# Performance work log

Hardware: AMD Instinct MI355X
Metric: run time of the kernel (lower is better)

Reference implementation:

```python
import jax, jax.numpy as jnp
import numpy as np

T_STEPS = 16
A = 64
B = 64
N = 16          # read_N
C = 3           # channels
H = 1024        # enc_size
IN = N * N * C  # LSTM input size = 768
EPS = 1e-8


def setup_inputs() -> dict:
    key = jax.random.key(0)
    ks = jax.random.split(key, 12)
    s = 0.02
    x = jax.random.normal(ks[0], (1024, C, B, A), dtype=jnp.float32)
    W_att = jax.random.normal(ks[1], (5, H), dtype=jnp.float32) * s
    b_att = jnp.zeros((5,), dtype=jnp.float32)
    W_ih = jax.random.normal(ks[2], (4 * H, IN), dtype=jnp.float32) * s
    W_hh = jax.random.normal(ks[3], (4 * H, H), dtype=jnp.float32) * s
    b_ih = jnp.zeros((4 * H,), dtype=jnp.float32)
    b_hh = jnp.zeros((4 * H,), dtype=jnp.float32)
    W_fc0 = jax.random.normal(ks[4], (H, H), dtype=jnp.float32) * s
    b_fc0 = jnp.zeros((H,), dtype=jnp.float32)
    W_fc = jax.random.normal(ks[5], (10, H), dtype=jnp.float32) * s
    b_fc = jnp.zeros((10,), dtype=jnp.float32)
    return {"x": x, "W_att": W_att, "b_att": b_att, "W_ih": W_ih, "W_hh": W_hh,
            "b_ih": b_ih, "b_hh": b_hh, "W_fc0": W_fc0, "b_fc0": b_fc0,
            "W_fc": W_fc, "b_fc": b_fc}


def _filterbank(gx, gy, sigma2, delta):
    # gx, gy, sigma2, delta: [Bt]
    grid = jnp.arange(N, dtype=jnp.float32)
    mu_x = gx[:, None] + (grid - N / 2 - 0.5) * delta[:, None]   # [Bt, N]
    mu_y = gy[:, None] + (grid - N / 2 - 0.5) * delta[:, None]   # [Bt, N]
    a = jnp.arange(A, dtype=jnp.float32)
    b = jnp.arange(B, dtype=jnp.float32)
    s2 = sigma2[:, None, None]
    Fx = jnp.exp(-(a[None, None, :] - mu_x[:, :, None]) ** 2 / (2 * s2))  # [Bt,N,A]
    Fy = jnp.exp(-(b[None, None, :] - mu_y[:, :, None]) ** 2 / (2 * s2))  # [Bt,N,B]
    Fx = Fx / (Fx.sum(2, keepdims=True) + EPS)
    Fy = Fy / (Fy.sum(2, keepdims=True) + EPS)
    return Fx, Fy


def _forward(x, W_att, b_att, W_ih, W_hh, b_ih, b_hh, W_fc0, b_fc0, W_fc, b_fc):
    Bt = x.shape[0]
    img = x.reshape(Bt, C, B, A)
    h0 = jnp.zeros((Bt, H), dtype=x.dtype)
    c0 = jnp.zeros((Bt, H), dtype=x.dtype)

    def step(carry, _):
        h, c = carry
        p = h @ W_att.T + b_att                      # [Bt, 5]
        gx_, gy_, log_s2, log_d, log_g = (p[:, 0], p[:, 1], p[:, 2], p[:, 3], p[:, 4])
        gx = (A + 1) / 2 * (gx_ + 1)
        gy = (B + 1) / 2 * (gy_ + 1)
        delta = (max(A, B) - 1) / (N - 1) * jnp.exp(log_d)
        sigma2 = jnp.exp(log_s2)
        gamma = jnp.exp(log_g)
        Fx, Fy = _filterbank(gx, gy, sigma2, delta)
        # glimpse[b,c] = Fy @ img[b,c] @ Fx^T -> [Bt, C, N, N]
        glimpse = jnp.einsum('bny,bcya,bxa->bcnx', Fy, img, Fx)
        r = glimpse.reshape(Bt, IN) * gamma[:, None]
        gates = r @ W_ih.T + b_ih + h @ W_hh.T + b_hh
        i_g, f_g, g_g, o_g = jnp.split(gates, 4, axis=1)
        c_new = jax.nn.sigmoid(f_g) * c + jax.nn.sigmoid(i_g) * jnp.tanh(g_g)
        h_new = jax.nn.sigmoid(o_g) * jnp.tanh(c_new)
        return (h_new, c_new), None

    (h, _), _ = jax.lax.scan(step, (h0, c0), None, length=T_STEPS)
    t = jax.nn.relu(h @ W_fc0.T + b_fc0)
    return t @ W_fc.T + b_fc


def reference(x, W_att, b_att, W_ih, W_hh, b_ih, b_hh, W_fc0, b_fc0, W_fc, b_fc):
    return _forward(x, W_att, b_att, W_ih, W_hh, b_ih, b_hh, W_fc0, b_fc0, W_fc, b_fc)
```

## Files before the change

kernel.cpp:

```cpp
#include <hip/hip_runtime.h>

typedef unsigned short u16;
typedef unsigned int u32;
typedef _Float16 f16;
typedef _Float16 half8 __attribute__((ext_vector_type(8)));
typedef _Float16 half4 __attribute__((ext_vector_type(4)));
typedef float f32x4 __attribute__((ext_vector_type(4)));

#define SPLIT_SC 2048.0f
#define SPLIT_INV (1.0f / 2048.0f)

__device__ __forceinline__ float sigf(float x) { return 1.0f / (1.0f + expf(-x)); }

__global__ __launch_bounds__(256) void att_glimpse(
    const f16* __restrict__ h_hi, const f16* __restrict__ h_lo,
    const float* __restrict__ Watt, const float* __restrict__ batt,
    const float* __restrict__ x,
    f16* __restrict__ r_hi, f16* __restrict__ r_lo)
{
    __shared__ float simg[64 * 64];
    __shared__ float sFx[16 * 68];
    __shared__ float sFyT[64 * 20];
    __shared__ float stmp[16 * 68];
    __shared__ float sred[4 * 5];
    __shared__ float spar[8];

    const int b = blockIdx.x, c = blockIdx.y, tid = threadIdx.x;
    const int lane = tid & 63, wave = tid >> 6;

    {
        const float4* src = (const float4*)(x + (size_t)b * 12288 + c * 4096);
        float4* dst = (float4*)simg;
        for (int i = tid; i < 1024; i += 256) dst[i] = src[i];
    }

    float p[5] = {0.f, 0.f, 0.f, 0.f, 0.f};
    {
        const f16* hh = h_hi + (size_t)b * 1024;
        const f16* hl = h_lo + (size_t)b * 1024;
        for (int k = tid; k < 1024; k += 256) {
            float hv = (float)hh[k] + (float)hl[k] * SPLIT_INV;
#pragma unroll
            for (int j = 0; j < 5; j++) p[j] += hv * Watt[j * 1024 + k];
        }
#pragma unroll
        for (int j = 0; j < 5; j++) {
#pragma unroll
            for (int o = 32; o > 0; o >>= 1) p[j] += __shfl_xor(p[j], o);
        }
        if (lane == 0) {
#pragma unroll
            for (int j = 0; j < 5; j++) sred[wave * 5 + j] = p[j];
        }
    }
    __syncthreads();
    if (tid == 0) {
        float q[5];
#pragma unroll
        for (int j = 0; j < 5; j++)
            q[j] = sred[j] + sred[5 + j] + sred[10 + j] + sred[15 + j] + batt[j];
        float q2 = fminf(fmaxf(q[2], -60.f), 60.f);
        float q3 = fminf(fmaxf(q[3], -60.f), 60.f);
        float q4 = fminf(fmaxf(q[4], -60.f), 60.f);
        spar[0] = 32.5f * (q[0] + 1.0f);
        spar[1] = 32.5f * (q[1] + 1.0f);
        spar[2] = 0.5f * expf(-q2);
        spar[3] = 4.2f * expf(q3);
        spar[4] = expf(q4);
    }
    __syncthreads();
    const float gx = spar[0], gy = spar[1], inv2s2 = spar[2], dl = spar[3],
                gamma = spar[4];

    {
        const float af = (float)lane;
#pragma unroll
        for (int i = 0; i < 4; i++) {
            int n = wave + i * 4;
            float nn = (float)n - 8.5f;
            float mux = gx + nn * dl;
            float ex = af - mux;
            float vx = expf(-ex * ex * inv2s2);
            float sx = vx;
#pragma unroll
            for (int o = 32; o > 0; o >>= 1) sx += __shfl_xor(sx, o);
            sFx[n * 68 + lane] = vx / (sx + 1e-8f);

            float muy = gy + nn * dl;
            float ey = af - muy;
            float vy = expf(-ey * ey * inv2s2);
            float sy = vy;
#pragma unroll
            for (int o = 32; o > 0; o >>= 1) sy += __shfl_xor(sy, o);
            sFyT[lane * 20 + n] = vy / (sy + 1e-8f);
        }
    }
    __syncthreads();

    {
        const int n4 = wave, ysub = lane >> 4, a4 = lane & 15;
        f32x4 acc[4];
#pragma unroll
        for (int j = 0; j < 4; j++) acc[j] = (f32x4)(0.f);
        for (int yy = 0; yy < 16; yy++) {
            int y = ysub * 16 + yy;
            float4 im = *(const float4*)(simg + y * 64 + a4 * 4);
            float4 fy = *(const float4*)(sFyT + y * 20 + n4 * 4);
            f32x4 iv = {im.x, im.y, im.z, im.w};
            acc[0] += fy.x * iv;
            acc[1] += fy.y * iv;
            acc[2] += fy.z * iv;
            acc[3] += fy.w * iv;
        }
#pragma unroll
        for (int j = 0; j < 4; j++) {
#pragma unroll
            for (int o = 16; o <= 32; o <<= 1) {
                acc[j].x += __shfl_xor(acc[j].x, o);
                acc[j].y += __shfl_xor(acc[j].y, o);
                acc[j].z += __shfl_xor(acc[j].z, o);
                acc[j].w += __shfl_xor(acc[j].w, o);
            }
        }
        if (ysub == 0) {
#pragma unroll
            for (int j = 0; j < 4; j++)
                *(f32x4*)(stmp + (n4 * 4 + j) * 68 + a4 * 4) = acc[j];
        }
    }
    __syncthreads();

    {
        const int n = tid >> 4, xo = tid & 15;
        const float* tp = stmp + n * 68;
        const float* fx = sFx + xo * 68;
        float s = 0.f;
        for (int a = 0; a < 64; a += 4) {
            float4 t4 = *(const float4*)(tp + a);
            float4 x4 = *(const float4*)(fx + a);
            s += t4.x * x4.x + t4.y * x4.y + t4.z * x4.z + t4.w * x4.w;
        }
        float v = s * gamma;
        f16 hi = (f16)v;
        size_t idx = (size_t)b * 768 + c * 256 + tid;
        r_hi[idx] = hi;
        r_lo[idx] = (f16)((v - (float)hi) * SPLIT_SC);
    }
}

__global__ __launch_bounds__(256) void swz_w(
    const float* __restrict__ W1, const float* __restrict__ W2,
    f16* __restrict__ out)
{
    const int kc = blockIdx.x >> 5, bn = blockIdx.x & 31;
    for (int t = threadIdx.x; t < 512; t += 256) {
        int c = t >> 6, lane = t & 63, l15 = lane & 15, lq = lane >> 4;
        int wrow = (c & 3) * 1024 + bn * 32 + l15 + ((c >> 2) << 4);
        const float* src;
        if (kc < 24) src = W1 + (size_t)wrow * 768 + kc * 32 + lq * 8;
        else         src = W2 + (size_t)wrow * 1024 + (kc - 24) * 32 + lq * 8;
        float4 g0 = *(const float4*)src;
        float4 g1 = *(const float4*)(src + 4);
        float gv[8] = {g0.x, g0.y, g0.z, g0.w, g1.x, g1.y, g1.z, g1.w};
        half8 hv, lv;
#pragma unroll
        for (int j = 0; j < 8; j++) {
            f16 h = (f16)gv[j];
            hv[j] = h;
            lv[j] = (f16)((gv[j] - (float)h) * SPLIT_SC);
        }
        size_t base = ((size_t)(kc * 32 + bn) * 16 + c * 2) * 512 + (size_t)lane * 8;
        *(half8*)(out + base) = hv;
        *(half8*)(out + base + 512) = lv;
    }
}

#define LDH 40

__global__ __launch_bounds__(256, 2) void gates_lstm(
    const f16* __restrict__ A1h, const f16* __restrict__ A1l,
    const f16* __restrict__ A2h, const f16* __restrict__ A2l,
    const f16* __restrict__ Wswz,
    const float* __restrict__ b1, const float* __restrict__ b2,
    float* __restrict__ cst,
    f16* __restrict__ Hh, f16* __restrict__ Hl)
{
    __shared__ f16 sA[2][2][64 * LDH];
    const int tid = threadIdx.x;
    const int kb = blockIdx.x;
    const int xcd = kb & 7, jb = kb >> 3;
    const int bn = xcd * 4 + (jb & 3);
    const int bm = jb >> 2;
    const int wave = tid >> 6, lane = tid & 63;
    const int wm = (wave >> 1) * 32;
    const int cbase = (wave & 1) * 4;
    const int l15 = lane & 15, lq = lane >> 4;
    const int arow = tid >> 2, acol = (tid & 3) * 8;

    f32x4 ah[2][4], al[2][4];
#pragma unroll
    for (int i = 0; i < 2; i++)
#pragma unroll
        for (int j = 0; j < 4; j++) { ah[i][j] = (f32x4)(0.f); al[i][j] = (f32x4)(0.f); }

    {
        size_t aoff = (size_t)(bm * 64 + arow) * 768 + acol;
        *(uint4*)&sA[0][0][arow * LDH + acol] = *(const uint4*)(A1h + aoff);
        *(uint4*)&sA[0][1][arow * LDH + acol] = *(const uint4*)(A1l + aoff);
    }
    half8 Bc[8];
    {
        const f16* wb = Wswz + (size_t)bn * 16 * 512 + (size_t)lane * 8;
#pragma unroll
        for (int nt = 0; nt < 4; nt++) {
            Bc[nt * 2]     = *(const half8*)(wb + (cbase + nt) * 1024);
            Bc[nt * 2 + 1] = *(const half8*)(wb + (cbase + nt) * 1024 + 512);
        }
    }

#pragma unroll 2
    for (int i = 0; i < 56; ++i) {
        const int cur = i & 1;
        __syncthreads();
        const int kn = (i + 1 < 56) ? i + 1 : 55;
        const f16 *pah, *pal; int astr, ako;
        if (kn < 24) { pah = A1h; pal = A1l; astr = 768;  ako = kn * 32; }
        else         { pah = A2h; pal = A2l; astr = 1024; ako = (kn - 24) * 32; }
        size_t aoff = (size_t)(bm * 64 + arow) * astr + ako + acol;
        uint4 vh = *(const uint4*)(pah + aoff);
        uint4 vl = *(const uint4*)(pal + aoff);
        half8 Bn[8];
        {
            const f16* wb = Wswz + (size_t)(kn * 32 + bn) * 16 * 512 + (size_t)lane * 8;
#pragma unroll
            for (int nt = 0; nt < 4; nt++) {
                Bn[nt * 2]     = *(const half8*)(wb + (cbase + nt) * 1024);
                Bn[nt * 2 + 1] = *(const half8*)(wb + (cbase + nt) * 1024 + 512);
            }
        }
        half8 afh[2], afl[2];
#pragma unroll
        for (int mt = 0; mt < 2; mt++) {
            int ro = (wm + mt * 16 + l15) * LDH + lq * 8;
            afh[mt] = *(const half8*)&sA[cur][0][ro];
            afl[mt] = *(const half8*)&sA[cur][1][ro];
        }
#pragma unroll
        for (int mt = 0; mt < 2; mt++)
#pragma unroll
            for (int nt = 0; nt < 4; nt++) {
                ah[mt][nt] = __builtin_amdgcn_mfma_f32_16x16x32_f16(
                    afh[mt], Bc[nt * 2], ah[mt][nt], 0, 0, 0);
                al[mt][nt] = __builtin_amdgcn_mfma_f32_16x16x32_f16(
                    afh[mt], Bc[nt * 2 + 1], al[mt][nt], 0, 0, 0);
                al[mt][nt] = __builtin_amdgcn_mfma_f32_16x16x32_f16(
                    afl[mt], Bc[nt * 2], al[mt][nt], 0, 0, 0);
            }
        const int nxt = cur ^ 1;
        *(uint4*)&sA[nxt][0][arow * LDH + acol] = vh;
        *(uint4*)&sA[nxt][1][arow * LDH + acol] = vl;
#pragma unroll
        for (int q = 0; q < 8; q++) Bc[q] = Bn[q];
    }

    const int u = bn * 32 + l15 + ((wave & 1) << 4);
    float bvs[4];
#pragma unroll
    for (int g = 0; g < 4; g++) bvs[g] = b1[g * 1024 + u] + b2[g * 1024 + u];
#pragma unroll
    for (int mt = 0; mt < 2; mt++) {
#pragma unroll
        for (int rg = 0; rg < 4; rg++) {
            int row = bm * 64 + wm + mt * 16 + lq * 4 + rg;
            size_t idx = (size_t)row * 1024 + u;
            float gi = ah[mt][0][rg] + al[mt][0][rg] * SPLIT_INV + bvs[0];
            float gf = ah[mt][1][rg] + al[mt][1][rg] * SPLIT_INV + bvs[1];
            float gg = ah[mt][2][rg] + al[mt][2][rg] * SPLIT_INV + bvs[2];
            float go = ah[mt][3][rg] + al[mt][3][rg] * SPLIT_INV + bvs[3];
            float cn = sigf(gf) * cst[idx] + sigf(gi) * tanhf(gg);
            float hn = sigf(go) * tanhf(cn);
            cst[idx] = cn;
            f16 hh = (f16)hn;
            Hh[idx] = hh;
            Hl[idx] = (f16)((hn - (float)hh) * SPLIT_SC);
        }
    }
}

__global__ __launch_bounds__(256) void fc0_gemm(
    const f16* __restrict__ Ah, const f16* __restrict__ Al,
    const float* __restrict__ W, const float* __restrict__ bias,
    float* __restrict__ out)
{
    __shared__ f16 sAh[64 * LDH], sAl[64 * LDH];
    __shared__ f16 sBh[64 * LDH], sBl[64 * LDH];
    const int tid = threadIdx.x;
    const int bm = blockIdx.x, bn = blockIdx.y;
    const int wave = tid >> 6, lane = tid & 63;
    const int wm = (wave >> 1) * 32, wn = (wave & 1) * 32;
    const int l15 = lane & 15, lq = lane >> 4;

    f32x4 ach[2][2], acx[2][2];
#pragma unroll
    for (int i = 0; i < 2; i++)
#pragma unroll
        for (int j = 0; j < 2; j++) { ach[i][j] = (f32x4)(0.f); acx[i][j] = (f32x4)(0.f); }

    for (int kc = 0; kc < 1024; kc += 32) {
        {
            int e = tid * 8;
            int row = e >> 5, col = e & 31;
            size_t off = (size_t)(bm * 64 + row) * 1024 + kc + col;
            *(uint4*)&sAh[row * LDH + col] = *(const uint4*)(Ah + off);
            *(uint4*)&sAl[row * LDH + col] = *(const uint4*)(Al + off);
        }
#pragma unroll
        for (int l = 0; l < 2; l++) {
            int e = (l * 256 + tid) * 4;
            int crow = e >> 5, col = e & 31;
            float4 g = *(const float4*)(W + (size_t)(bn * 64 + crow) * 1024 + kc + col);
            f16 h0 = (f16)g.x, h1 = (f16)g.y, h2 = (f16)g.z, h3 = (f16)g.w;
            half4 hv = {h0, h1, h2, h3};
            half4 lv = {(f16)((g.x - (float)h0) * SPLIT_SC),
                        (f16)((g.y - (float)h1) * SPLIT_SC),
                        (f16)((g.z - (float)h2) * SPLIT_SC),
                        (f16)((g.w - (float)h3) * SPLIT_SC)};
            *(half4*)&sBh[crow * LDH + col] = hv;
            *(half4*)&sBl[crow * LDH + col] = lv;
        }
        __syncthreads();
        half8 afh[2], afl[2], bfh[2], bfl[2];
#pragma unroll
        for (int mt = 0; mt < 2; mt++) {
            int ro = (wm + mt * 16 + l15) * LDH + lq * 8;
            afh[mt] = *(const half8*)&sAh[ro];
            afl[mt] = *(const half8*)&sAl[ro];
        }
#pragma unroll
        for (int nt = 0; nt < 2; nt++) {
            int ro = (wn + nt * 16 + l15) * LDH + lq * 8;
            bfh[nt] = *(const half8*)&sBh[ro];
            bfl[nt] = *(const half8*)&sBl[ro];
        }
#pragma unroll
        for (int mt = 0; mt < 2; mt++)
#pragma unroll
            for (int nt = 0; nt < 2; nt++) {
                ach[mt][nt] = __builtin_amdgcn_mfma_f32_16x16x32_f16(
                    afh[mt], bfh[nt], ach[mt][nt], 0, 0, 0);
                acx[mt][nt] = __builtin_amdgcn_mfma_f32_16x16x32_f16(
                    afh[mt], bfl[nt], acx[mt][nt], 0, 0, 0);
                acx[mt][nt] = __builtin_amdgcn_mfma_f32_16x16x32_f16(
                    afl[mt], bfh[nt], acx[mt][nt], 0, 0, 0);
            }
        __syncthreads();
    }

#pragma unroll
    for (int mt = 0; mt < 2; mt++) {
#pragma unroll
        for (int nt = 0; nt < 2; nt++) {
            int col = bn * 64 + wn + nt * 16 + l15;
            float bv = bias[col];
#pragma unroll
            for (int rg = 0; rg < 4; rg++) {
                int row = bm * 64 + wm + mt * 16 + lq * 4 + rg;
                float v = ach[mt][nt][rg] + acx[mt][nt][rg] * SPLIT_INV + bv;
                out[(size_t)row * 1024 + col] = fmaxf(v, 0.f);
            }
        }
    }
}

__global__ __launch_bounds__(64) void fc_out(
    const float* __restrict__ tb, const float* __restrict__ Wfc,
    const float* __restrict__ bfc, float* __restrict__ out)
{
    int b = blockIdx.x, lane = threadIdx.x;
    const float* tv = tb + (size_t)b * 1024;
    float p[10];
#pragma unroll
    for (int j = 0; j < 10; j++) p[j] = 0.f;
    for (int k = lane; k < 1024; k += 64) {
        float t = tv[k];
#pragma unroll
        for (int j = 0; j < 10; j++) p[j] += t * Wfc[j * 1024 + k];
    }
#pragma unroll
    for (int j = 0; j < 10; j++) {
#pragma unroll
        for (int o = 32; o > 0; o >>= 1) p[j] += __shfl_xor(p[j], o);
    }
    if (lane == 0) {
#pragma unroll
        for (int j = 0; j < 10; j++) out[b * 10 + j] = p[j] + bfc[j];
    }
}

extern "C" void kernel_launch(void* const* d_in, const int* in_sizes, int n_in,
                              void* d_out, int out_size, void* d_ws, size_t ws_size,
                              hipStream_t stream)
{
    const float* x     = (const float*)d_in[0];
    const float* W_att = (const float*)d_in[1];
    const float* b_att = (const float*)d_in[2];
    const float* W_ih  = (const float*)d_in[3];
    const float* W_hh  = (const float*)d_in[4];
    const float* b_ih  = (const float*)d_in[5];
    const float* b_hh  = (const float*)d_in[6];
    const float* W_fc0 = (const float*)d_in[7];
    const float* b_fc0 = (const float*)d_in[8];
    const float* W_fc  = (const float*)d_in[9];
    const float* b_fc  = (const float*)d_in[10];
    float* out = (float*)d_out;

    char* ws = (char*)d_ws;
    f16*   Wswz   = (f16*)ws;    ws += (size_t)56 * 32 * 16 * 512 * 2;
    float* c_f32  = (float*)ws;  ws += (size_t)1024 * 1024 * 4;
    f16*   h_hi0  = (f16*)ws;    ws += (size_t)1024 * 1024 * 2;
    f16*   h_hi1  = (f16*)ws;    ws += (size_t)1024 * 1024 * 2;
    f16*   h_lo0  = (f16*)ws;    ws += (size_t)1024 * 1024 * 2;
    f16*   h_lo1  = (f16*)ws;    ws += (size_t)1024 * 1024 * 2;
    f16*   r_hi   = (f16*)ws;    ws += (size_t)1024 * 768 * 2;
    f16*   r_lo   = (f16*)ws;    ws += (size_t)1024 * 768 * 2;
    float* t_f32  = c_f32;
    f16* h_hi[2] = {h_hi0, h_hi1};
    f16* h_lo[2] = {h_lo0, h_lo1};

    hipMemsetAsync(c_f32, 0, (size_t)1024 * 1024 * 4, stream);
    hipMemsetAsync(h_hi0, 0, (size_t)1024 * 1024 * 2, stream);
    hipMemsetAsync(h_lo0, 0, (size_t)1024 * 1024 * 2, stream);

    swz_w<<<56 * 32, 256, 0, stream>>>(W_ih, W_hh, Wswz);

    for (int t = 0; t < 16; t++) {
        int rb = t & 1, wb = 1 - rb;
        att_glimpse<<<dim3(1024, 3), 256, 0, stream>>>(
            h_hi[rb], h_lo[rb], W_att, b_att, x, r_hi, r_lo);
        gates_lstm<<<512, 256, 0, stream>>>(
            r_hi, r_lo, h_hi[rb], h_lo[rb], Wswz, b_ih, b_hh,
            c_f32, h_hi[wb], h_lo[wb]);
    }
    fc0_gemm<<<dim3(16, 16), 256, 0, stream>>>(
        h_hi[0], h_lo[0], W_fc0, b_fc0, t_f32);
    fc_out<<<1024, 64, 0, stream>>>(t_f32, W_fc, b_fc, out);
}
```

Baseline: 1.462 ms.

## Re-tile LSTM gate GEMM so each wave covers all rows with interleaved gate columns

The weight swizzle now interleaves gate columns so each 16-wide MFMA column tile holds two gates for 8 hidden units. Each wave covers all 64 rows and 2 column tiles instead of 32 rows and 4 tiles. This halves per-wave B-fragment global loads and doubles LDS A-fragment reads. The epilogue exchanges gate values across lanes with shuffles, and only half the lanes do the LSTM cell update.

```diff
diff --git a/kernel.cpp b/kernel.cpp
--- a/kernel.cpp
+++ b/kernel.cpp
@@ -155,7 +155,9 @@
     const int kc = blockIdx.x >> 5, bn = blockIdx.x & 31;
     for (int t = threadIdx.x; t < 512; t += 256) {
         int c = t >> 6, lane = t & 63, l15 = lane & 15, lq = lane >> 4;
-        int wrow = (c & 3) * 1024 + bn * 32 + l15 + ((c >> 2) << 4);
+        int gate = ((c & 1) << 1) + (l15 >> 3);
+        int ul   = ((c >> 1) << 3) + (l15 & 7);
+        int wrow = gate * 1024 + bn * 32 + ul;
         const float* src;
         if (kc < 24) src = W1 + (size_t)wrow * 768 + kc * 32 + lq * 8;
         else         src = W2 + (size_t)wrow * 1024 + (kc - 24) * 32 + lq * 8;
@@ -192,27 +194,26 @@
     const int bn = xcd * 4 + (jb & 3);
     const int bm = jb >> 2;
     const int wave = tid >> 6, lane = tid & 63;
-    const int wm = (wave >> 1) * 32;
-    const int cbase = (wave & 1) * 4;
+    const int cbase = wave * 2;
     const int l15 = lane & 15, lq = lane >> 4;
     const int arow = tid >> 2, acol = (tid & 3) * 8;
 
-    f32x4 ah[2][4], al[2][4];
-#pragma unroll
-    for (int i = 0; i < 2; i++)
-#pragma unroll
-        for (int j = 0; j < 4; j++) { ah[i][j] = (f32x4)(0.f); al[i][j] = (f32x4)(0.f); }
+    f32x4 ah[4][2], al[4][2];
+#pragma unroll
+    for (int i = 0; i < 4; i++)
+#pragma unroll
+        for (int j = 0; j < 2; j++) { ah[i][j] = (f32x4)(0.f); al[i][j] = (f32x4)(0.f); }
 
     {
         size_t aoff = (size_t)(bm * 64 + arow) * 768 + acol;
         *(uint4*)&sA[0][0][arow * LDH + acol] = *(const uint4*)(A1h + aoff);
         *(uint4*)&sA[0][1][arow * LDH + acol] = *(const uint4*)(A1l + aoff);
     }
-    half8 Bc[8];
+    half8 Bc[4];
     {
         const f16* wb = Wswz + (size_t)bn * 16 * 512 + (size_t)lane * 8;
 #pragma unroll
-        for (int nt = 0; nt < 4; nt++) {
+        for (int nt = 0; nt < 2; nt++) {
             Bc[nt * 2]     = *(const half8*)(wb + (cbase + nt) * 1024);
             Bc[nt * 2 + 1] = *(const half8*)(wb + (cbase + nt) * 1024 + 512);
         }
@@ -229,26 +230,26 @@
         size_t aoff = (size_t)(bm * 64 + arow) * astr + ako + acol;
         uint4 vh = *(const uint4*)(pah + aoff);
         uint4 vl = *(const uint4*)(pal + aoff);
-        half8 Bn[8];
+        half8 Bn[4];
         {
             const f16* wb = Wswz + (size_t)(kn * 32 + bn) * 16 * 512 + (size_t)lane * 8;
 #pragma unroll
-            for (int nt = 0; nt < 4; nt++) {
+            for (int nt = 0; nt < 2; nt++) {
                 Bn[nt * 2]     = *(const half8*)(wb + (cbase + nt) * 1024);
                 Bn[nt * 2 + 1] = *(const half8*)(wb + (cbase + nt) * 1024 + 512);
             }
         }
-        half8 afh[2], afl[2];
-#pragma unroll
-        for (int mt = 0; mt < 2; mt++) {
-            int ro = (wm + mt * 16 + l15) * LDH + lq * 8;
+        half8 afh[4], afl[4];
+#pragma unroll
+        for (int mt = 0; mt < 4; mt++) {
+            int ro = (mt * 16 + l15) * LDH + lq * 8;
             afh[mt] = *(const half8*)&sA[cur][0][ro];
             afl[mt] = *(const half8*)&sA[cur][1][ro];
         }
 #pragma unroll
-        for (int mt = 0; mt < 2; mt++)
-#pragma unroll
-            for (int nt = 0; nt < 4; nt++) {
+        for (int mt = 0; mt < 4; mt++)
+#pragma unroll
+            for (int nt = 0; nt < 2; nt++) {
                 ah[mt][nt] = __builtin_amdgcn_mfma_f32_16x16x32_f16(
                     afh[mt], Bc[nt * 2], ah[mt][nt], 0, 0, 0);
                 al[mt][nt] = __builtin_amdgcn_mfma_f32_16x16x32_f16(
@@ -260,29 +261,35 @@
         *(uint4*)&sA[nxt][0][arow * LDH + acol] = vh;
         *(uint4*)&sA[nxt][1][arow * LDH + acol] = vl;
 #pragma unroll
-        for (int q = 0; q < 8; q++) Bc[q] = Bn[q];
-    }
-
-    const int u = bn * 32 + l15 + ((wave & 1) << 4);
-    float bvs[4];
-#pragma unroll
-    for (int g = 0; g < 4; g++) bvs[g] = b1[g * 1024 + u] + b2[g * 1024 + u];
-#pragma unroll
-    for (int mt = 0; mt < 2; mt++) {
+        for (int q = 0; q < 4; q++) Bc[q] = Bn[q];
+    }
+
+    const int g0 = l15 >> 3;
+    const int u = bn * 32 + wave * 8 + (l15 & 7);
+    const float bv0 = b1[g0 * 1024 + u] + b2[g0 * 1024 + u];
+    const float bv1 = b1[(g0 + 2) * 1024 + u] + b2[(g0 + 2) * 1024 + u];
+#pragma unroll
+    for (int mt = 0; mt < 4; mt++) {
 #pragma unroll
         for (int rg = 0; rg < 4; rg++) {
-            int row = bm * 64 + wm + mt * 16 + lq * 4 + rg;
+            int row = bm * 64 + mt * 16 + lq * 4 + rg;
             size_t idx = (size_t)row * 1024 + u;
-            float gi = ah[mt][0][rg] + al[mt][0][rg] * SPLIT_INV + bvs[0];
-            float gf = ah[mt][1][rg] + al[mt][1][rg] * SPLIT_INV + bvs[1];
-            float gg = ah[mt][2][rg] + al[mt][2][rg] * SPLIT_INV + bvs[2];
-            float go = ah[mt][3][rg] + al[mt][3][rg] * SPLIT_INV + bvs[3];
-            float cn = sigf(gf) * cst[idx] + sigf(gi) * tanhf(gg);
-            float hn = sigf(go) * tanhf(cn);
-            cst[idx] = cn;
-            f16 hh = (f16)hn;
-            Hh[idx] = hh;
-            Hl[idx] = (f16)((hn - (float)hh) * SPLIT_SC);
+            float mine0 = ah[mt][0][rg] + al[mt][0][rg] * SPLIT_INV + bv0;
+            float mine1 = ah[mt][1][rg] + al[mt][1][rg] * SPLIT_INV + bv1;
+            float oth0 = __shfl_xor(mine0, 8);
+            float oth1 = __shfl_xor(mine1, 8);
+            float gi = (g0 == 0) ? mine0 : oth0;
+            float gg = (g0 == 0) ? mine1 : oth1;
+            float gf = (g0 == 0) ? oth0 : mine0;
+            float go = (g0 == 0) ? oth1 : mine1;
+            if (g0 == 0) {
+                float cn = sigf(gf) * cst[idx] + sigf(gi) * tanhf(gg);
+                float hn = sigf(go) * tanhf(cn);
+                cst[idx] = cn;
+                f16 hh = (f16)hn;
+                Hh[idx] = hh;
+                Hl[idx] = (f16)((hn - (float)hh) * SPLIT_SC);
+            }
         }
     }
 }
```

Result: no change. 1.464 ms (+0.2%).
